# Optimization experiments

Hardware: AMD Instinct MI355X
Metric: run time of the kernel (lower is better)

## Reference

```python
import jax, jax.numpy as jnp
import numpy as np

N, E, NFEAT, NHID, K, TOP_N, NCLASS = 50000, 800000, 512, 128, 4, 2, 64
ALPHA = 0.2   # LeakyReLU negative slope (config.alpha)
EPS = 1e-16   # avoid 0/0 for isolated / fully-masked nodes


def _spgat_layer(h, src, dst, a, mask, concat):
    """SpGraphAttentionLayer_2: attention over given edges, no internal W.
    h: (N, F); a: (2F,); mask: optional (E,) 0/1 edge-subset mask.
    edge_e = exp(-leakyrelu(a . [h_src; h_dst]));
    out = segsum(e * h_dst) / segsum(e)  (per target node src).
    """
    F = h.shape[1]
    s1 = h @ a[:F]                     # (N,)
    s2 = h @ a[F:]                     # (N,)
    e = jnp.exp(-jax.nn.leaky_relu(s1[src] + s2[dst], ALPHA))  # (E,)
    if mask is not None:
        e = e * mask
    rowsum = jax.ops.segment_sum(e, src, num_segments=N)              # (N,)
    hp = jax.ops.segment_sum(e[:, None] * h[dst], src, num_segments=N)  # (N,F)
    hp = hp / (rowsum[:, None] + EPS)
    return jax.nn.elu(hp) if concat else hp


def setup_inputs() -> dict:
    key = jax.random.key(0)
    ks = jax.random.split(key, 7)
    x = jax.random.normal(ks[0], (N, NFEAT), jnp.float32)
    edge = jax.random.randint(ks[1], (2, E), 0, N)
    W_ks = jax.random.normal(ks[2], (K, NFEAT, NHID), jnp.float32) * 0.05
    a_k = jax.random.normal(ks[3], (K, 2 * NHID * K), jnp.float32) * 0.05
    W_o = jax.random.normal(ks[4], (NHID * K, NCLASS), jnp.float32) * 0.05
    a_att = jax.random.normal(ks[5], (K, 2 * NHID), jnp.float32) * 0.05
    a_out = jax.random.normal(ks[6], (2 * NCLASS,), jnp.float32) * 0.05
    return {"x": x, "edge": edge, "W_ks": W_ks, "a_k": a_k,
            "W_o": W_o, "a_att": a_att, "a_out": a_out}


def reference(x, edge, W_ks, a_k, W_o, a_att, a_out):
    src, dst = edge[0], edge[1]
    # K per-factor projections; dropout is a no-op in eval mode
    h_k = jnp.einsum('nf,kfh->knh', x, W_ks)              # (K, N, H)
    h = jnp.transpose(h_k, (1, 0, 2)).reshape(N, K * NHID)  # cat(h_k, dim=1)
    # Edge-level factor routing: softmax_K( a_k @ [h_src; h_dst] ).
    # Linear score => precompute per-node halves instead of (E, 2KH) gather.
    s_src = h @ a_k[:, :K * NHID].T                       # (N, K)
    s_dst = h @ a_k[:, K * NHID:].T                       # (N, K)
    edge_att = jax.nn.softmax(s_src[src] + s_dst[dst], axis=-1)  # (E, K)
    top_att, top_idx = jax.lax.top_k(edge_att, TOP_N)     # (E, TOP_N)
    # edge e belongs to factor k iff k is among its top_n factors
    masks = (top_idx[:, :, None] == jnp.arange(K)[None, None, :]).any(1)  # (E, K)
    outs = [_spgat_layer(h_k[k], src, dst, a_att[k],
                         masks[:, k].astype(h.dtype), True) for k in range(K)]
    xo = jnp.concatenate(outs, axis=1) @ W_o              # (N, NCLASS)
    xo = jax.nn.elu(_spgat_layer(xo, src, dst, a_out, None, False))
    att_loss = jnp.mean(1.0 - jnp.sum(top_att, axis=1))
    return jax.nn.log_softmax(xo, axis=1), att_loss
```

## Files before the change

### kernel.cpp

```cpp
#include <hip/hip_runtime.h>
#include <math.h>

#define NN 50000
#define NE 800000
#define NF 512
#define NH 128
#define KF 4
#define NC 64
#define LRELU_ALPHA 0.2f
#define EPSF 1e-16f

typedef unsigned short u16;
typedef __attribute__((ext_vector_type(8))) short bf16x8;
typedef __attribute__((ext_vector_type(4))) float f32x4;

#define OFF_H      0LL
#define OFF_HP     (OFF_H + (long long)NN * NF)
#define OFF_REC    (OFF_HP + (long long)NN * NF)
#define OFF_XO0    (OFF_REC + 4LL * NE)
#define OFF_SSRC   (OFF_XO0 + (long long)NN * NC)
#define OFF_SDST   (OFF_SSRC + (long long)NN * KF)
#define OFF_S1A    (OFF_SDST + (long long)NN * KF)
#define OFF_S2A    (OFF_S1A + (long long)NN * KF)
#define OFF_WOT    (OFF_S2A + (long long)NN * KF)
#define OFF_S1O    (OFF_WOT + (long long)NN * KF)
#define OFF_S2O    (OFF_S1O + NN)
#define OFF_START  (OFF_S2O + NN)
#define OFF_CNT    (OFF_START + NN + 4)
#define OFF_CURSOR (OFF_CNT + NN)
#define OFF_ATT    (OFF_CURSOR + NN)
#define WS_FLOATS  (OFF_ATT + 2)

__device__ __forceinline__ u16 bf16_rne(float f) {
    unsigned int u = __float_as_uint(f);
    return (u16)((u + 0x7FFFu + ((u >> 16) & 1u)) >> 16);
}
__device__ __forceinline__ float bf16_f(u16 b) {
    return __uint_as_float(((unsigned int)b) << 16);
}

__device__ __forceinline__ void gload_lds16(const u16* g, u16* l) {
    __builtin_amdgcn_global_load_lds(
        (const __attribute__((address_space(1))) void*)g,
        (__attribute__((address_space(3))) void*)l, 16, 0, 0);
}

#define NSPLIT 12500
__global__ __launch_bounds__(256) void split_x_count(
        const float* __restrict__ x, u16* __restrict__ xhi, u16* __restrict__ xlo,
        const int* __restrict__ edge, int* __restrict__ cnt) {
    if (blockIdx.x < NSPLIT) {
        size_t i = ((size_t)blockIdx.x * 256 + threadIdx.x) * 8;
        float4 v0 = *(const float4*)(x + i);
        float4 v1 = *(const float4*)(x + i + 4);
        float v[8] = {v0.x, v0.y, v0.z, v0.w, v1.x, v1.y, v1.z, v1.w};
        unsigned int hp[4], lp[4];
#pragma unroll
        for (int j = 0; j < 4; ++j) {
            u16 h0 = bf16_rne(v[2 * j]);
            u16 h1 = bf16_rne(v[2 * j + 1]);
            u16 l0 = bf16_rne(v[2 * j] - bf16_f(h0));
            u16 l1 = bf16_rne(v[2 * j + 1] - bf16_f(h1));
            hp[j] = (unsigned int)h0 | ((unsigned int)h1 << 16);
            lp[j] = (unsigned int)l0 | ((unsigned int)l1 << 16);
        }
        *(uint4*)(xhi + i) = make_uint4(hp[0], hp[1], hp[2], hp[3]);
        *(uint4*)(xlo + i) = make_uint4(lp[0], lp[1], lp[2], lp[3]);
    } else {
        int e = (blockIdx.x - NSPLIT) * 256 + threadIdx.x;
        if (e < NE) atomicAdd(&cnt[edge[e]], 1);
    }
}

__global__ void split_w(const float* __restrict__ Wks, const float* __restrict__ Wo,
                        u16* __restrict__ wthi, u16* __restrict__ wtlo,
                        u16* __restrict__ wohi, u16* __restrict__ wolo) {
    int b = blockIdx.x;
    if (b < 512) {
        int kf = b >> 7, n = b & 127;
        for (int f = threadIdx.x; f < NF; f += 256) {
            float v = Wks[(size_t)kf * (NF * NH) + (size_t)f * NH + n];
            u16 hb = bf16_rne(v);
            u16 lb = bf16_rne(v - bf16_f(hb));
            wthi[(size_t)b * NF + f] = hb;
            wtlo[(size_t)b * NF + f] = lb;
        }
    } else {
        int n = b - 512;
        for (int f = threadIdx.x; f < NF; f += 256) {
            float v = Wo[(size_t)f * NC + n];
            u16 hb = bf16_rne(v);
            u16 lb = bf16_rne(v - bf16_f(hb));
            wohi[(size_t)n * NF + f] = hb;
            wolo[(size_t)n * NF + f] = lb;
        }
    }
}

__global__ __launch_bounds__(256) void gemm_h_mfma(
        const u16* __restrict__ xhi, const u16* __restrict__ xlo,
        const u16* __restrict__ wthi, const u16* __restrict__ wtlo,
        float* __restrict__ h) {
    __shared__ u16 Ah[128 * 32], Al[128 * 32], Bh[128 * 32], Bl[128 * 32];
    const int nwg = 4 * ((NN + 127) / 128);
    const int q = nwg / 8, r = nwg % 8;
    int o = blockIdx.x;
    int xcd = o & 7, pos = o >> 3;
    int wg = (xcd < r ? xcd * (q + 1) : r * (q + 1) + (xcd - r) * q) + pos;
    int m0 = (wg >> 2) * 128, n0 = (wg & 3) * 128;

    int tid = threadIdx.x;
    int lane = tid & 63;
    int wave = tid >> 6, wm = wave >> 1, wn = wave & 1;
    f32x4 acc[4][4];
#pragma unroll
    for (int i = 0; i < 4; ++i)
#pragma unroll
        for (int j = 0; j < 4; ++j) acc[i][j] = (f32x4)(0.f);

    u16* sbuf = (wave == 0) ? Ah : (wave == 1) ? Al : (wave == 2) ? Bh : Bl;
    const u16* gbase = (wave == 0) ? xhi : (wave == 1) ? xlo
                     : (wave == 2) ? wthi : wtlo;
    int rowbase = (wave < 2) ? m0 : n0;
    int c16s = (lane & 3) ^ ((lane >> 2) & 3) ^ (lane >> 4);
    const u16* gsrc[8];
#pragma unroll
    for (int i = 0; i < 8; ++i) {
        int rowg = rowbase + 16 * i + (lane >> 2);
        if (wave < 2 && rowg >= NN) rowg = NN - 1;
        gsrc[i] = gbase + (size_t)rowg * NF + c16s * 8;
    }

    const int arow = wm * 64 + (lane & 15);
    const int brow = wn * 64 + (lane & 15);
    const int rc16 = (lane >> 4) ^ ((lane & 3) ^ ((lane >> 2) & 3));
    const int fragoff = rc16 * 8;

    for (int k0 = 0; k0 < NF; k0 += 32) {
        __syncthreads();
#pragma unroll
        for (int i = 0; i < 8; ++i)
            gload_lds16(gsrc[i] + k0, sbuf + i * 512);
        __syncthreads();
        bf16x8 ah[4], al[4], bh[4], bl[4];
#pragma unroll
        for (int mi = 0; mi < 4; ++mi) {
            ah[mi] = *(const bf16x8*)(Ah + (arow + mi * 16) * 32 + fragoff);
            al[mi] = *(const bf16x8*)(Al + (arow + mi * 16) * 32 + fragoff);
        }
#pragma unroll
        for (int ni = 0; ni < 4; ++ni) {
            bh[ni] = *(const bf16x8*)(Bh + (brow + ni * 16) * 32 + fragoff);
            bl[ni] = *(const bf16x8*)(Bl + (brow + ni * 16) * 32 + fragoff);
        }
#pragma unroll
        for (int mi = 0; mi < 4; ++mi)
#pragma unroll
            for (int ni = 0; ni < 4; ++ni) {
                acc[mi][ni] = __builtin_amdgcn_mfma_f32_16x16x32_bf16(
                    ah[mi], bh[ni], acc[mi][ni], 0, 0, 0);
                acc[mi][ni] = __builtin_amdgcn_mfma_f32_16x16x32_bf16(
                    ah[mi], bl[ni], acc[mi][ni], 0, 0, 0);
                acc[mi][ni] = __builtin_amdgcn_mfma_f32_16x16x32_bf16(
                    al[mi], bh[ni], acc[mi][ni], 0, 0, 0);
            }
    }
#pragma unroll
    for (int mi = 0; mi < 4; ++mi) {
        int mbase = m0 + wm * 64 + mi * 16 + (lane >> 4) * 4;
#pragma unroll
        for (int ni = 0; ni < 4; ++ni) {
            int n = n0 + wn * 64 + ni * 16 + (lane & 15);
#pragma unroll
            for (int r2 = 0; r2 < 4; ++r2) {
                int m = mbase + r2;
                if (m < NN) h[(size_t)m * NF + n] = acc[mi][ni][r2];
            }
        }
    }
}

__global__ __launch_bounds__(256) void compute_svals_h(
        const float* __restrict__ h, const float* __restrict__ a_k,
        const float* __restrict__ a_att,
        float* __restrict__ s_src, float* __restrict__ s_dst,
        float* __restrict__ s1a, float* __restrict__ s2a) {
    __shared__ float Ak[4][1024];
    __shared__ float Aa[4][256];
    for (int i = threadIdx.x; i < 4096; i += 256) Ak[i >> 10][i & 1023] = a_k[i];
    for (int i = threadIdx.x; i < 1024; i += 256) Aa[i >> 8][i & 255] = a_att[i];
    __syncthreads();
    int w = threadIdx.x >> 6, lane = threadIdx.x & 63;
    for (int n = blockIdx.x * 4 + w; n < NN; n += gridDim.x * 4) {
        const float* hr = h + (size_t)n * NF;
        float accS[4] = {0, 0, 0, 0}, accD[4] = {0, 0, 0, 0};
        float accQ1[4] = {0, 0, 0, 0}, accQ2[4] = {0, 0, 0, 0};
#pragma unroll
        for (int i = 0; i < 8; ++i) {
            int f = i * 64 + lane;
            float hv = hr[f];
#pragma unroll
            for (int k = 0; k < 4; ++k) {
                accS[k] = fmaf(hv, Ak[k][f], accS[k]);
                accD[k] = fmaf(hv, Ak[k][512 + f], accD[k]);
            }
            accQ1[i >> 1] = fmaf(hv, Aa[i >> 1][f & 127], accQ1[i >> 1]);
            accQ2[i >> 1] = fmaf(hv, Aa[i >> 1][128 + (f & 127)], accQ2[i >> 1]);
        }
#pragma unroll
        for (int off = 32; off >= 1; off >>= 1) {
#pragma unroll
            for (int k = 0; k < 4; ++k) {
                accS[k] += __shfl_xor(accS[k], off);
                accD[k] += __shfl_xor(accD[k], off);
                accQ1[k] += __shfl_xor(accQ1[k], off);
                accQ2[k] += __shfl_xor(accQ2[k], off);
            }
        }
        if (lane == 0) {
#pragma unroll
            for (int k = 0; k < 4; ++k) {
                s_src[n * 4 + k] = accS[k];
                s_dst[n * 4 + k] = accD[k];
                s1a[n * 4 + k]   = accQ1[k];
                s2a[n * 4 + k]   = accQ2[k];
            }
        }
    }
}

__global__ __launch_bounds__(1024) void csr_scan(const int* __restrict__ cnt,
                                                 int* __restrict__ start) {
    __shared__ int part[1024];
    int t = threadIdx.x;
    const int CH = (NN + 1023) / 1024;
    int base = t * CH;
    int s = 0;
    for (int i = 0; i < CH; ++i) {
        int idx = base + i;
        if (idx < NN) s += cnt[idx];
    }
    part[t] = s;
    __syncthreads();
    for (int off = 1; off < 1024; off <<= 1) {
        int v = (t >= off) ? part[t - off] : 0;
        __syncthreads();
        part[t] += v;
        __syncthreads();
    }
    int run = (t == 0) ? 0 : part[t - 1];
    for (int i = 0; i < CH; ++i) {
        int idx = base + i;
        if (idx < NN) { start[idx] = run; run += cnt[idx]; }
    }
    if (t == 1023) start[NN] = run;
}

__global__ __launch_bounds__(256) void edge_pre1(
        const int* __restrict__ edge, const int* __restrict__ start,
        int* __restrict__ cursor,
        const float* __restrict__ s_src, const float* __restrict__ s_dst,
        const float* __restrict__ s1a, const float* __restrict__ s2a,
        int4* __restrict__ rec, double* __restrict__ att_acc) {
    __shared__ float blk[4];
    int tid = threadIdx.x;
    int e = blockIdx.x * 256 + tid;
    float t2 = 0.f;
    if (e < NE) {
        int src = edge[e];
        int dst = edge[NE + e];
        float4 ss = *(const float4*)(s_src + (size_t)src * 4);
        float4 sd = *(const float4*)(s_dst + (size_t)dst * 4);
        float l0 = ss.x + sd.x, l1 = ss.y + sd.y, l2 = ss.z + sd.z, l3 = ss.w + sd.w;
        int i1 = 0; float v1 = l0;
        if (l1 > v1) { v1 = l1; i1 = 1; }
        if (l2 > v1) { v1 = l2; i1 = 2; }
        if (l3 > v1) { v1 = l3; i1 = 3; }
        int i2 = 0; float v2 = -3.4e38f;
        if (i1 != 0)            { v2 = l0; i2 = 0; }
        if (i1 != 1 && l1 > v2) { v2 = l1; i2 = 1; }
        if (i1 != 2 && l2 > v2) { v2 = l2; i2 = 2; }
        if (i1 != 3 && l3 > v2) { v2 = l3; i2 = 3; }
        float esum = expf(l0 - v1) + expf(l1 - v1) + expf(l2 - v1) + expf(l3 - v1);
        t2 = (1.f + expf(v2 - v1)) / esum;
        float4 q1 = *(const float4*)(s1a + (size_t)src * 4);
        float4 q2 = *(const float4*)(s2a + (size_t)dst * 4);
        float q1v1 = i1 == 0 ? q1.x : i1 == 1 ? q1.y : i1 == 2 ? q1.z : q1.w;
        float q2v1 = i1 == 0 ? q2.x : i1 == 1 ? q2.y : i1 == 2 ? q2.z : q2.w;
        float q1v2 = i2 == 0 ? q1.x : i2 == 1 ? q1.y : i2 == 2 ? q1.z : q1.w;
        float q2v2 = i2 == 0 ? q2.x : i2 == 1 ? q2.y : i2 == 2 ? q2.z : q2.w;
        float sv1 = q1v1 + q2v1, sv2 = q1v2 + q2v2;
        float ee1 = expf(-(sv1 >= 0.f ? sv1 : LRELU_ALPHA * sv1));
        float ee2 = expf(-(sv2 >= 0.f ? sv2 : LRELU_ALPHA * sv2));
        int p = start[src] + atomicAdd(&cursor[src], 1);
        rec[p] = make_int4(dst, src | (i1 << 16) | (i2 << 18),
                           __float_as_int(ee1), __float_as_int(ee2));
    }
#pragma unroll
    for (int off = 32; off >= 1; off >>= 1) t2 += __shfl_xor(t2, off);
    if ((tid & 63) == 0) blk[tid >> 6] = t2;
    __syncthreads();
    if (tid == 0)
        atomicAdd(att_acc, (double)(blk[0] + blk[1] + blk[2] + blk[3]));
}

__global__ __launch_bounds__(256) void node_gather1(
        const int* __restrict__ start, const int4* __restrict__ rec,
        const float* __restrict__ h,
        u16* __restrict__ ahi, u16* __restrict__ alo) {
    __shared__ float red[4][512];
    __shared__ float rsred[4][4];
    int n = blockIdx.x;
    int w = threadIdx.x >> 6, lane = threadIdx.x & 63;
    int j0 = start[n], j1 = start[n + 1];
    float a00 = 0.f, a01 = 0.f, a10 = 0.f, a11 = 0.f;
    float a20 = 0.f, a21 = 0.f, a30 = 0.f, a31 = 0.f;
    float rs0 = 0.f, rs1 = 0.f, rs2 = 0.f, rs3 = 0.f;
    for (int j = j0 + w; j < j1; j += 4) {
        int4 r = rec[j];
        int i1 = (r.y >> 16) & 3, i2 = (r.y >> 18) & 3;
        float w1 = __int_as_float(r.z), w2 = __int_as_float(r.w);
        const float* hr = h + (size_t)r.x * NF + lane;
        float v1a = hr[i1 * 128];
        float v1b = hr[i1 * 128 + 64];
        float v2a = hr[i2 * 128];
        float v2b = hr[i2 * 128 + 64];
        switch (i1) {
            case 0: a00 = fmaf(w1, v1a, a00); a01 = fmaf(w1, v1b, a01); rs0 += w1; break;
            case 1: a10 = fmaf(w1, v1a, a10); a11 = fmaf(w1, v1b, a11); rs1 += w1; break;
            case 2: a20 = fmaf(w1, v1a, a20); a21 = fmaf(w1, v1b, a21); rs2 += w1; break;
            default:a30 = fmaf(w1, v1a, a30); a31 = fmaf(w1, v1b, a31); rs3 += w1; break;
        }
        switch (i2) {
            case 0: a00 = fmaf(w2, v2a, a00); a01 = fmaf(w2, v2b, a01); rs0 += w2; break;
            case 1: a10 = fmaf(w2, v2a, a10); a11 = fmaf(w2, v2b, a11); rs1 += w2; break;
            case 2: a20 = fmaf(w2, v2a, a20); a21 = fmaf(w2, v2b, a21); rs2 += w2; break;
            default:a30 = fmaf(w2, v2a, a30); a31 = fmaf(w2, v2b, a31); rs3 += w2; break;
        }
    }
    red[w][lane]       = a00; red[w][64 + lane]  = a01;
    red[w][128 + lane] = a10; red[w][192 + lane] = a11;
    red[w][256 + lane] = a20; red[w][320 + lane] = a21;
    red[w][384 + lane] = a30; red[w][448 + lane] = a31;
    if (lane == 0) {
        rsred[w][0] = rs0; rsred[w][1] = rs1; rsred[w][2] = rs2; rsred[w][3] = rs3;
    }
    __syncthreads();
    int t = threadIdx.x;
    float s0 = (red[0][t] + red[1][t]) + (red[2][t] + red[3][t]);
    float s1 = (red[0][256 + t] + red[1][256 + t]) + (red[2][256 + t] + red[3][256 + t]);
    int f0 = t >> 7, f1 = 2 + (t >> 7);
    float rsa = (rsred[0][f0] + rsred[1][f0]) + (rsred[2][f0] + rsred[3][f0]) + EPSF;
    float rsb = (rsred[0][f1] + rsred[1][f1]) + (rsred[2][f1] + rsred[3][f1]) + EPSF;
    float e0 = s0 / rsa; e0 = e0 > 0.f ? e0 : expm1f(e0);
    float e1 = s1 / rsb; e1 = e1 > 0.f ? e1 : expm1f(e1);
    u16 h0 = bf16_rne(e0), l0 = bf16_rne(e0 - bf16_f(h0));
    u16 h1 = bf16_rne(e1), l1 = bf16_rne(e1 - bf16_f(h1));
    u16* ah = ahi + (size_t)n * NF;
    u16* al = alo + (size_t)n * NF;
    ah[t] = h0; ah[256 + t] = h1;
    al[t] = l0; al[256 + t] = l1;
}

__global__ __launch_bounds__(256) void node_pass_mfma(
        const u16* __restrict__ ahi, const u16* __restrict__ alo,
        const u16* __restrict__ wohi, const u16* __restrict__ wolo,
        float* __restrict__ xo0) {
    __shared__ u16 Ah[128 * 32], Al[128 * 32], Bh[64 * 32], Bl[64 * 32];
    int m0 = blockIdx.x * 128;
    int tid = threadIdx.x;
    int lane = tid & 63;
    int wave = tid >> 6, wm = wave >> 1, wn = wave & 1;
    f32x4 acc[4][2];
#pragma unroll
    for (int i = 0; i < 4; ++i)
#pragma unroll
        for (int j = 0; j < 2; ++j) acc[i][j] = (f32x4)(0.f);

    u16* sbuf = (wave == 0) ? Ah : (wave == 1) ? Al : (wave == 2) ? Bh : Bl;
    const u16* gbase = (wave == 0) ? ahi : (wave == 1) ? alo
                     : (wave == 2) ? wohi : wolo;
    int nld = (wave < 2) ? 8 : 4;
    int c16s = (lane & 3) ^ ((lane >> 2) & 3) ^ (lane >> 4);
    const u16* gsrc[8];
#pragma unroll
    for (int i = 0; i < 8; ++i) {
        int rowg = ((wave < 2) ? m0 : 0) + 16 * i + (lane >> 2);
        if (wave < 2 && rowg >= NN) rowg = NN - 1;
        gsrc[i] = gbase + (size_t)rowg * NF + c16s * 8;
    }

    const int arow = wm * 64 + (lane & 15);
    const int brow = wn * 32 + (lane & 15);
    const int rc16 = (lane >> 4) ^ ((lane & 3) ^ ((lane >> 2) & 3));
    const int fragoff = rc16 * 8;

    for (int k0 = 0; k0 < NF; k0 += 32) {
        __syncthreads();
        for (int i = 0; i < nld; ++i)
            gload_lds16(gsrc[i] + k0, sbuf + i * 512);
        __syncthreads();
        bf16x8 ah[4], al[4], bh[2], bl[2];
#pragma unroll
        for (int mi = 0; mi < 4; ++mi) {
            ah[mi] = *(const bf16x8*)(Ah + (arow + mi * 16) * 32 + fragoff);
            al[mi] = *(const bf16x8*)(Al + (arow + mi * 16) * 32 + fragoff);
        }
#pragma unroll
        for (int ni = 0; ni < 2; ++ni) {
            bh[ni] = *(const bf16x8*)(Bh + (brow + ni * 16) * 32 + fragoff);
            bl[ni] = *(const bf16x8*)(Bl + (brow + ni * 16) * 32 + fragoff);
        }
#pragma unroll
        for (int mi = 0; mi < 4; ++mi)
#pragma unroll
            for (int ni = 0; ni < 2; ++ni) {
                acc[mi][ni] = __builtin_amdgcn_mfma_f32_16x16x32_bf16(
                    ah[mi], bh[ni], acc[mi][ni], 0, 0, 0);
                acc[mi][ni] = __builtin_amdgcn_mfma_f32_16x16x32_bf16(
                    ah[mi], bl[ni], acc[mi][ni], 0, 0, 0);
                acc[mi][ni] = __builtin_amdgcn_mfma_f32_16x16x32_bf16(
                    al[mi], bh[ni], acc[mi][ni], 0, 0, 0);
            }
    }
#pragma unroll
    for (int mi = 0; mi < 4; ++mi) {
        int mbase = m0 + wm * 64 + mi * 16 + (lane >> 4) * 4;
#pragma unroll
        for (int ni = 0; ni < 2; ++ni) {
            int n = wn * 32 + ni * 16 + (lane & 15);
#pragma unroll
            for (int r2 = 0; r2 < 4; ++r2) {
                int m = mbase + r2;
                if (m < NN) xo0[(size_t)m * NC + n] = acc[mi][ni][r2];
            }
        }
    }
}

__global__ __launch_bounds__(256) void dots_out(
        const float* __restrict__ xo0, const float* __restrict__ a_out,
        const double* __restrict__ att_acc,
        float* __restrict__ s1o, float* __restrict__ s2o, float* __restrict__ out) {
    if (blockIdx.x == 0 && threadIdx.x == 0)
        out[(size_t)NN * NC] = 1.f - (float)(att_acc[0] / (double)NE);
    int w = threadIdx.x >> 6, lane = threadIdx.x & 63;
    int n = blockIdx.x * 4 + w;
    if (n >= NN) return;
    float v = xo0[(size_t)n * NC + lane];
    float p1 = v * a_out[lane];
    float p2 = v * a_out[64 + lane];
#pragma unroll
    for (int off = 32; off >= 1; off >>= 1) {
        p1 += __shfl_xor(p1, off);
        p2 += __shfl_xor(p2, off);
    }
    if (lane == 0) { s1o[n] = p1; s2o[n] = p2; }
}

__global__ __launch_bounds__(256) void node_gather2(
        const int* __restrict__ start, const int4* __restrict__ rec,
        const float* __restrict__ s1o, const float* __restrict__ s2o,
        const float* __restrict__ xo0, float* __restrict__ out) {
    __shared__ float red[4][64];
    __shared__ float rsl[4];
    int n = blockIdx.x;
    int w = threadIdx.x >> 6, lane = threadIdx.x & 63;
    int j0 = start[n], j1 = start[n + 1];
    float s1n = s1o[n];
    float acc = 0.f, rsum = 0.f;
    for (int j = j0 + w; j < j1; j += 4) {
        int d = rec[j].x;
        float sv = s1n + s2o[d];
        float e = expf(-(sv >= 0.f ? sv : LRELU_ALPHA * sv));
        acc = fmaf(e, xo0[(size_t)d * NC + lane], acc);
        rsum += e;
    }
    red[w][lane] = acc;
    if (lane == 0) rsl[w] = rsum;
    __syncthreads();
    if (w == 0) {
        float a = (red[0][lane] + red[1][lane]) + (red[2][lane] + red[3][lane]);
        float r = (rsl[0] + rsl[1]) + (rsl[2] + rsl[3]);
        float t = a / (r + EPSF);
        float v = t > 0.f ? t : expm1f(t);
        float m = v;
#pragma unroll
        for (int off = 32; off >= 1; off >>= 1) m = fmaxf(m, __shfl_xor(m, off));
        float p = expf(v - m);
#pragma unroll
        for (int off = 32; off >= 1; off >>= 1) p += __shfl_xor(p, off);
        out[(size_t)n * NC + lane] = v - m - logf(p);
    }
}

extern "C" void kernel_launch(void* const* d_in, const int* in_sizes, int n_in,
                              void* d_out, int out_size, void* d_ws, size_t ws_size,
                              hipStream_t stream) {
    const float* x     = (const float*)d_in[0];
    const int*   edge  = (const int*)d_in[1];
    const float* Wks   = (const float*)d_in[2];
    const float* a_k   = (const float*)d_in[3];
    const float* Wo    = (const float*)d_in[4];
    const float* a_att = (const float*)d_in[5];
    const float* a_out = (const float*)d_in[6];
    float* out = (float*)d_out;

    float* wsf = (float*)d_ws;
    float* h      = wsf + OFF_H;
    int4*  rec    = (int4*)(wsf + OFF_REC);
    float* xo0    = wsf + OFF_XO0;
    float* s_src  = wsf + OFF_SSRC;
    float* s_dst  = wsf + OFF_SDST;
    float* s1a    = wsf + OFF_S1A;
    float* s2a    = wsf + OFF_S2A;
    float* s1o    = wsf + OFF_S1O;
    float* s2o    = wsf + OFF_S2O;
    int*   startp = (int*)(wsf + OFF_START);
    int*   cnt    = (int*)(wsf + OFF_CNT);
    int*   cursor = (int*)(wsf + OFF_CURSOR);
    double* att   = (double*)(wsf + OFF_ATT);

    u16* xhi  = (u16*)(wsf + OFF_HP);
    u16* xlo  = xhi + (size_t)NN * NF;
    u16* ahi  = xhi;
    u16* alo  = xlo;
    u16* wthi = (u16*)(wsf + OFF_REC);
    u16* wtlo = wthi + (size_t)KF * NH * NF;
    u16* wohi = (u16*)(wsf + OFF_WOT);
    u16* wolo = wohi + (size_t)NC * NF;

    size_t zero_bytes = (size_t)(WS_FLOATS - OFF_CNT) * sizeof(float);
    hipMemsetAsync((char*)d_ws + (size_t)OFF_CNT * sizeof(float), 0, zero_bytes, stream);

    split_x_count<<<NSPLIT + (NE + 255) / 256, 256, 0, stream>>>(x, xhi, xlo, edge, cnt);
    split_w<<<512 + NC, 256, 0, stream>>>(Wks, Wo, wthi, wtlo, wohi, wolo);
    csr_scan<<<1, 1024, 0, stream>>>(cnt, startp);
    gemm_h_mfma<<<4 * ((NN + 127) / 128), 256, 0, stream>>>(xhi, xlo, wthi, wtlo, h);
    compute_svals_h<<<256, 256, 0, stream>>>(h, a_k, a_att, s_src, s_dst, s1a, s2a);
    edge_pre1<<<(NE + 255) / 256, 256, 0, stream>>>(edge, startp, cursor,
                                                    s_src, s_dst, s1a, s2a, rec, att);
    node_gather1<<<NN, 256, 0, stream>>>(startp, rec, h, ahi, alo);
    node_pass_mfma<<<(NN + 127) / 128, 256, 0, stream>>>(ahi, alo, wohi, wolo, xo0);
    dots_out<<<(NN + 3) / 4, 256, 0, stream>>>(xo0, a_out, att, s1o, s2o, out);
    node_gather2<<<NN, 256, 0, stream>>>(startp, rec, s1o, s2o, xo0, out);
}
```

Baseline: 647.9 us.

## Fuse setup kernels, fold output dots into MFMA epilogue, unroll gathers

Merges the weight-split kernel into the x-split/count kernel, which removes one launch. The attention dot products for the output layer are now computed in the node_pass_mfma epilogue, so dots_out and its extra read of xo0 go away. The att_loss write moves into node_gather2. The two gather loops are unrolled by two so each wave has two independent record loads and row gathers in flight, at the cost of more register pressure.

```diff
diff --git a/kernel.cpp b/kernel.cpp
--- a/kernel.cpp
+++ b/kernel.cpp
@@ -46,9 +46,13 @@
 }
 
 #define NSPLIT 12500
-__global__ __launch_bounds__(256) void split_x_count(
+#define NCNT   ((NE + 255) / 256)
+__global__ __launch_bounds__(256) void split_all(
         const float* __restrict__ x, u16* __restrict__ xhi, u16* __restrict__ xlo,
-        const int* __restrict__ edge, int* __restrict__ cnt) {
+        const int* __restrict__ edge, int* __restrict__ cnt,
+        const float* __restrict__ Wks, const float* __restrict__ Wo,
+        u16* __restrict__ wthi, u16* __restrict__ wtlo,
+        u16* __restrict__ wohi, u16* __restrict__ wolo) {
     if (blockIdx.x < NSPLIT) {
         size_t i = ((size_t)blockIdx.x * 256 + threadIdx.x) * 8;
         float4 v0 = *(const float4*)(x + i);
@@ -66,33 +70,29 @@
         }
         *(uint4*)(xhi + i) = make_uint4(hp[0], hp[1], hp[2], hp[3]);
         *(uint4*)(xlo + i) = make_uint4(lp[0], lp[1], lp[2], lp[3]);
-    } else {
+    } else if (blockIdx.x < NSPLIT + NCNT) {
         int e = (blockIdx.x - NSPLIT) * 256 + threadIdx.x;
         if (e < NE) atomicAdd(&cnt[edge[e]], 1);
-    }
-}
-
-__global__ void split_w(const float* __restrict__ Wks, const float* __restrict__ Wo,
-                        u16* __restrict__ wthi, u16* __restrict__ wtlo,
-                        u16* __restrict__ wohi, u16* __restrict__ wolo) {
-    int b = blockIdx.x;
-    if (b < 512) {
-        int kf = b >> 7, n = b & 127;
-        for (int f = threadIdx.x; f < NF; f += 256) {
-            float v = Wks[(size_t)kf * (NF * NH) + (size_t)f * NH + n];
-            u16 hb = bf16_rne(v);
-            u16 lb = bf16_rne(v - bf16_f(hb));
-            wthi[(size_t)b * NF + f] = hb;
-            wtlo[(size_t)b * NF + f] = lb;
-        }
     } else {
-        int n = b - 512;
-        for (int f = threadIdx.x; f < NF; f += 256) {
-            float v = Wo[(size_t)f * NC + n];
-            u16 hb = bf16_rne(v);
-            u16 lb = bf16_rne(v - bf16_f(hb));
-            wohi[(size_t)n * NF + f] = hb;
-            wolo[(size_t)n * NF + f] = lb;
+        int b = blockIdx.x - NSPLIT - NCNT;
+        if (b < 512) {
+            int kf = b >> 7, n = b & 127;
+            for (int f = threadIdx.x; f < NF; f += 256) {
+                float v = Wks[(size_t)kf * (NF * NH) + (size_t)f * NH + n];
+                u16 hb = bf16_rne(v);
+                u16 lb = bf16_rne(v - bf16_f(hb));
+                wthi[(size_t)b * NF + f] = hb;
+                wtlo[(size_t)b * NF + f] = lb;
+            }
+        } else {
+            int n = b - 512;
+            for (int f = threadIdx.x; f < NF; f += 256) {
+                float v = Wo[(size_t)f * NC + n];
+                u16 hb = bf16_rne(v);
+                u16 lb = bf16_rne(v - bf16_f(hb));
+                wohi[(size_t)n * NF + f] = hb;
+                wolo[(size_t)n * NF + f] = lb;
+            }
         }
     }
 }
@@ -304,6 +304,28 @@
         atomicAdd(att_acc, (double)(blk[0] + blk[1] + blk[2] + blk[3]));
 }
 
+#define G1_BODY(RR)                                                             \
+    {   int i1 = ((RR).y >> 16) & 3, i2 = ((RR).y >> 18) & 3;                   \
+        float w1 = __int_as_float((RR).z), w2 = __int_as_float((RR).w);         \
+        const float* hr = h + (size_t)(RR).x * NF + lane;                       \
+        float v1a = hr[i1 * 128];                                               \
+        float v1b = hr[i1 * 128 + 64];                                          \
+        float v2a = hr[i2 * 128];                                               \
+        float v2b = hr[i2 * 128 + 64];                                          \
+        switch (i1) {                                                           \
+            case 0: a00 = fmaf(w1, v1a, a00); a01 = fmaf(w1, v1b, a01); rs0 += w1; break; \
+            case 1: a10 = fmaf(w1, v1a, a10); a11 = fmaf(w1, v1b, a11); rs1 += w1; break; \
+            case 2: a20 = fmaf(w1, v1a, a20); a21 = fmaf(w1, v1b, a21); rs2 += w1; break; \
+            default:a30 = fmaf(w1, v1a, a30); a31 = fmaf(w1, v1b, a31); rs3 += w1; break; \
+        }                                                                       \
+        switch (i2) {                                                           \
+            case 0: a00 = fmaf(w2, v2a, a00); a01 = fmaf(w2, v2b, a01); rs0 += w2; break; \
+            case 1: a10 = fmaf(w2, v2a, a10); a11 = fmaf(w2, v2b, a11); rs1 += w2; break; \
+            case 2: a20 = fmaf(w2, v2a, a20); a21 = fmaf(w2, v2b, a21); rs2 += w2; break; \
+            default:a30 = fmaf(w2, v2a, a30); a31 = fmaf(w2, v2b, a31); rs3 += w2; break; \
+        }                                                                       \
+    }
+
 __global__ __launch_bounds__(256) void node_gather1(
         const int* __restrict__ start, const int4* __restrict__ rec,
         const float* __restrict__ h,
@@ -316,27 +338,16 @@
     float a00 = 0.f, a01 = 0.f, a10 = 0.f, a11 = 0.f;
     float a20 = 0.f, a21 = 0.f, a30 = 0.f, a31 = 0.f;
     float rs0 = 0.f, rs1 = 0.f, rs2 = 0.f, rs3 = 0.f;
-    for (int j = j0 + w; j < j1; j += 4) {
-        int4 r = rec[j];
-        int i1 = (r.y >> 16) & 3, i2 = (r.y >> 18) & 3;
-        float w1 = __int_as_float(r.z), w2 = __int_as_float(r.w);
-        const float* hr = h + (size_t)r.x * NF + lane;
-        float v1a = hr[i1 * 128];
-        float v1b = hr[i1 * 128 + 64];
-        float v2a = hr[i2 * 128];
-        float v2b = hr[i2 * 128 + 64];
-        switch (i1) {
-            case 0: a00 = fmaf(w1, v1a, a00); a01 = fmaf(w1, v1b, a01); rs0 += w1; break;
-            case 1: a10 = fmaf(w1, v1a, a10); a11 = fmaf(w1, v1b, a11); rs1 += w1; break;
-            case 2: a20 = fmaf(w1, v1a, a20); a21 = fmaf(w1, v1b, a21); rs2 += w1; break;
-            default:a30 = fmaf(w1, v1a, a30); a31 = fmaf(w1, v1b, a31); rs3 += w1; break;
-        }
-        switch (i2) {
-            case 0: a00 = fmaf(w2, v2a, a00); a01 = fmaf(w2, v2b, a01); rs0 += w2; break;
-            case 1: a10 = fmaf(w2, v2a, a10); a11 = fmaf(w2, v2b, a11); rs1 += w2; break;
-            case 2: a20 = fmaf(w2, v2a, a20); a21 = fmaf(w2, v2b, a21); rs2 += w2; break;
-            default:a30 = fmaf(w2, v2a, a30); a31 = fmaf(w2, v2b, a31); rs3 += w2; break;
-        }
+    int j = j0 + w;
+    for (; j + 4 < j1; j += 8) {
+        int4 ra = rec[j];
+        int4 rb = rec[j + 4];
+        G1_BODY(ra)
+        G1_BODY(rb)
+    }
+    if (j < j1) {
+        int4 ra = rec[j];
+        G1_BODY(ra)
     }
     red[w][lane]       = a00; red[w][64 + lane]  = a01;
     red[w][128 + lane] = a10; red[w][192 + lane] = a11;
@@ -365,8 +376,11 @@
 __global__ __launch_bounds__(256) void node_pass_mfma(
         const u16* __restrict__ ahi, const u16* __restrict__ alo,
         const u16* __restrict__ wohi, const u16* __restrict__ wolo,
-        float* __restrict__ xo0) {
+        const float* __restrict__ a_out,
+        float* __restrict__ xo0, float* __restrict__ s1o, float* __restrict__ s2o) {
     __shared__ u16 Ah[128 * 32], Al[128 * 32], Bh[64 * 32], Bl[64 * 32];
+    __shared__ float part1[2][64][2];
+    __shared__ float part2[2][64][2];
     int m0 = blockIdx.x * 128;
     int tid = threadIdx.x;
     int lane = tid & 63;
@@ -436,40 +450,70 @@
             }
         }
     }
-}
-
-__global__ __launch_bounds__(256) void dots_out(
-        const float* __restrict__ xo0, const float* __restrict__ a_out,
-        const double* __restrict__ att_acc,
-        float* __restrict__ s1o, float* __restrict__ s2o, float* __restrict__ out) {
-    if (blockIdx.x == 0 && threadIdx.x == 0)
-        out[(size_t)NN * NC] = 1.f - (float)(att_acc[0] / (double)NE);
-    int w = threadIdx.x >> 6, lane = threadIdx.x & 63;
-    int n = blockIdx.x * 4 + w;
-    if (n >= NN) return;
-    float v = xo0[(size_t)n * NC + lane];
-    float p1 = v * a_out[lane];
-    float p2 = v * a_out[64 + lane];
-#pragma unroll
-    for (int off = 32; off >= 1; off >>= 1) {
-        p1 += __shfl_xor(p1, off);
-        p2 += __shfl_xor(p2, off);
-    }
-    if (lane == 0) { s1o[n] = p1; s2o[n] = p2; }
+    float ao1[2], ao2[2];
+#pragma unroll
+    for (int ni = 0; ni < 2; ++ni) {
+        int c = wn * 32 + ni * 16 + (lane & 15);
+        ao1[ni] = a_out[c];
+        ao2[ni] = a_out[64 + c];
+    }
+#pragma unroll
+    for (int mi = 0; mi < 4; ++mi)
+#pragma unroll
+        for (int r2 = 0; r2 < 4; ++r2) {
+            float p1 = acc[mi][0][r2] * ao1[0] + acc[mi][1][r2] * ao1[1];
+            float p2 = acc[mi][0][r2] * ao2[0] + acc[mi][1][r2] * ao2[1];
+#pragma unroll
+            for (int off = 8; off >= 1; off >>= 1) {
+                p1 += __shfl_xor(p1, off);
+                p2 += __shfl_xor(p2, off);
+            }
+            if ((lane & 15) == 0) {
+                int rl = mi * 16 + (lane >> 4) * 4 + r2;
+                part1[wm][rl][wn] = p1;
+                part2[wm][rl][wn] = p2;
+            }
+        }
+    __syncthreads();
+    if (tid < 128) {
+        int m = m0 + tid;
+        if (m < NN) {
+            s1o[m] = part1[tid >> 6][tid & 63][0] + part1[tid >> 6][tid & 63][1];
+            s2o[m] = part2[tid >> 6][tid & 63][0] + part2[tid >> 6][tid & 63][1];
+        }
+    }
 }
 
 __global__ __launch_bounds__(256) void node_gather2(
         const int* __restrict__ start, const int4* __restrict__ rec,
         const float* __restrict__ s1o, const float* __restrict__ s2o,
-        const float* __restrict__ xo0, float* __restrict__ out) {
+        const float* __restrict__ xo0, const double* __restrict__ att_acc,
+        float* __restrict__ out) {
     __shared__ float red[4][64];
     __shared__ float rsl[4];
+    if (blockIdx.x == 0 && threadIdx.x == 0)
+        out[(size_t)NN * NC] = 1.f - (float)(att_acc[0] / (double)NE);
     int n = blockIdx.x;
     int w = threadIdx.x >> 6, lane = threadIdx.x & 63;
     int j0 = start[n], j1 = start[n + 1];
     float s1n = s1o[n];
     float acc = 0.f, rsum = 0.f;
-    for (int j = j0 + w; j < j1; j += 4) {
+    int j = j0 + w;
+    for (; j + 4 < j1; j += 8) {
+        int da = rec[j].x;
+        int db = rec[j + 4].x;
+        float sva = s1n + s2o[da];
+        float svb = s1n + s2o[db];
+        float ea = expf(-(sva >= 0.f ? sva : LRELU_ALPHA * sva));
+        float eb = expf(-(svb >= 0.f ? svb : LRELU_ALPHA * svb));
+        float xa = xo0[(size_t)da * NC + lane];
+        float xb = xo0[(size_t)db * NC + lane];
+        acc = fmaf(ea, xa, acc);
+        rsum += ea;
+        acc = fmaf(eb, xb, acc);
+        rsum += eb;
+    }
+    if (j < j1) {
         int d = rec[j].x;
         float sv = s1n + s2o[d];
         float e = expf(-(sv >= 0.f ? sv : LRELU_ALPHA * sv));
@@ -533,15 +577,15 @@
     size_t zero_bytes = (size_t)(WS_FLOATS - OFF_CNT) * sizeof(float);
     hipMemsetAsync((char*)d_ws + (size_t)OFF_CNT * sizeof(float), 0, zero_bytes, stream);
 
-    split_x_count<<<NSPLIT + (NE + 255) / 256, 256, 0, stream>>>(x, xhi, xlo, edge, cnt);
-    split_w<<<512 + NC, 256, 0, stream>>>(Wks, Wo, wthi, wtlo, wohi, wolo);
+    split_all<<<NSPLIT + NCNT + 576, 256, 0, stream>>>(
+        x, xhi, xlo, edge, cnt, Wks, Wo, wthi, wtlo, wohi, wolo);
     csr_scan<<<1, 1024, 0, stream>>>(cnt, startp);
     gemm_h_mfma<<<4 * ((NN + 127) / 128), 256, 0, stream>>>(xhi, xlo, wthi, wtlo, h);
     compute_svals_h<<<256, 256, 0, stream>>>(h, a_k, a_att, s_src, s_dst, s1a, s2a);
     edge_pre1<<<(NE + 255) / 256, 256, 0, stream>>>(edge, startp, cursor,
                                                     s_src, s_dst, s1a, s2a, rec, att);
     node_gather1<<<NN, 256, 0, stream>>>(startp, rec, h, ahi, alo);
-    node_pass_mfma<<<(NN + 127) / 128, 256, 0, stream>>>(ahi, alo, wohi, wolo, xo0);
-    dots_out<<<(NN + 3) / 4, 256, 0, stream>>>(xo0, a_out, att, s1o, s2o, out);
-    node_gather2<<<NN, 256, 0, stream>>>(startp, rec, s1o, s2o, xo0, out);
-}
+    node_pass_mfma<<<(NN + 127) / 128, 256, 0, stream>>>(ahi, alo, wohi, wolo,
+                                                         a_out, xo0, s1o, s2o);
+    node_gather2<<<NN, 256, 0, stream>>>(startp, rec, s1o, s2o, xo0, att, out);
+}
```

Result: faster. 606.5 us (-6.4%).
